# Kernel tuning notes

Hardware: AMD Instinct MI355X
Metric: run time of the kernel (lower is better)

Reference implementation:

```python
import jax, jax.numpy as jnp
import numpy as np

N = 50000      # nodes
K = 32         # fixed neighbor count per node
D_IN, D_HID, D_OUT = 512, 128, 64


def setup_inputs() -> dict:
    key = jax.random.key(0)
    k1, k2, k3, k4 = jax.random.split(key, 4)
    feat = jax.random.normal(k1, (N, D_IN), dtype=jnp.float32)
    W1 = jax.random.normal(k2, (D_IN, D_HID), dtype=jnp.float32) * (1.0 / np.sqrt(D_IN))
    b1 = jnp.zeros((D_HID,), dtype=jnp.float32)
    W2 = jax.random.normal(k3, (D_HID, D_OUT), dtype=jnp.float32) * (1.0 / np.sqrt(D_HID))
    b2 = jnp.zeros((D_OUT,), dtype=jnp.float32)
    neighbors = jax.random.randint(k4, (N, K), 0, N, dtype=jnp.int64)
    return {"feat": feat, "W1": W1, "b1": b1, "W2": W2, "b2": b2,
            "neighbors": neighbors}


def _median_conv(x, W, b, neighbors):
    # linear transform, then per-node median over neighbor messages
    h = x @ W + b                      # [N, D]
    nb = h[neighbors]                  # [N, K, D]  gather (irregular access)
    # torch.median returns the lower middle element for even K
    med = jnp.sort(nb, axis=1)[:, (K - 1) // 2]   # [N, D]
    return med


def reference(feat, W1, b1, W2, b2, neighbors):
    # MedianGCN forward (eval mode: dropout is identity), norm='none'
    h = jax.nn.relu(_median_conv(feat, W1, b1, neighbors))
    out = _median_conv(h, W2, b2, neighbors)
    return out
```

## Files before the change

### kernel.cpp

```cpp
#include <hip/hip_runtime.h>
#include <cstddef>

#define NN   50000
#define KNB  32

typedef _Float16 h2    __attribute__((ext_vector_type(2)));
typedef _Float16 half8 __attribute__((ext_vector_type(8)));
typedef float    f4    __attribute__((ext_vector_type(4)));
typedef float    f8    __attribute__((ext_vector_type(8)));

__global__ __launch_bounds__(256) void prep(const float* __restrict__ W1,
                                            const float* __restrict__ W2,
                                            _Float16* __restrict__ w1t,
                                            _Float16* __restrict__ w2t) {
  const int id = blockIdx.x * 256 + threadIdx.x;
  if (id < 128 * 512) {
    const int n = id >> 9, k = id & 511;
    w1t[id] = (_Float16)W1[k * 128 + n];
  } else {
    const int id2 = id - 128 * 512;
    if (id2 < 64 * 128) {
      const int n = id2 >> 7, k = id2 & 127;
      w2t[id2] = (_Float16)W2[k * 64 + n];
    }
  }
}

__global__ __launch_bounds__(256) void gemm1_mfma(
    const float* __restrict__ A, const _Float16* __restrict__ Bt,
    const float* __restrict__ bias, _Float16* __restrict__ C, int M) {
  constexpr int K = 512, BM = 64, BK = 32;
  __shared__ _Float16 Ah[BM][40];
  __shared__ _Float16 Bh[128][40];
  const int tid  = threadIdx.x;
  const int wave = tid >> 6;
  const int lane = tid & 63;
  const int mr   = lane & 15;
  const int kg   = lane >> 4;
  const int m0   = blockIdx.x * BM;

  const int srow = tid >> 2;
  const int sseg = (tid & 3) * 8;
  int aRow = m0 + srow;
  if (aRow >= M) aRow = M - 1;
  const float*    ap  = A  + (size_t)aRow * K + sseg;
  const _Float16* bp0 = Bt + (size_t)srow * K + sseg;
  const _Float16* bp1 = Bt + (size_t)(64 + srow) * K + sseg;

  f4 acc[8] = {};

  for (int k0 = 0; k0 < K; k0 += BK) {
    const f4 t0 = *(const f4*)ap;
    const f4 t1 = *(const f4*)(ap + 4);
    const half8 blo = *(const half8*)bp0;
    const half8 bhi = *(const half8*)bp1;
    const f8 av = {t0[0], t0[1], t0[2], t0[3], t1[0], t1[1], t1[2], t1[3]};
    *(half8*)&Ah[srow][sseg]      = __builtin_convertvector(av, half8);
    *(half8*)&Bh[srow][sseg]      = blo;
    *(half8*)&Bh[64 + srow][sseg] = bhi;
    __syncthreads();

    const half8 af = *(const half8*)&Ah[wave * 16 + mr][kg * 8];
    #pragma unroll
    for (int nt = 0; nt < 8; ++nt) {
      const half8 bf = *(const half8*)&Bh[nt * 16 + mr][kg * 8];
      acc[nt] = __builtin_amdgcn_mfma_f32_16x16x32_f16(af, bf, acc[nt], 0, 0, 0);
    }
    __syncthreads();
    ap += BK;
    bp0 += BK;
    bp1 += BK;
  }

  #pragma unroll
  for (int nt = 0; nt < 8; ++nt) {
    const int col = nt * 16 + mr;
    const float bv = bias[col];
    #pragma unroll
    for (int r = 0; r < 4; ++r) {
      const int row = m0 + wave * 16 + kg * 4 + r;
      if (row < M)
        C[(size_t)row * 128 + col] = (_Float16)(acc[nt][r] + bv);
    }
  }
}

__global__ __launch_bounds__(256) void gemm2_mfma(
    const _Float16* __restrict__ A, const _Float16* __restrict__ Bt,
    const float* __restrict__ bias, _Float16* __restrict__ C, int M) {
  constexpr int K = 128, BM = 64, BK = 32;
  __shared__ _Float16 Ah[BM][40];
  __shared__ _Float16 Bh[64][40];
  const int tid  = threadIdx.x;
  const int wave = tid >> 6;
  const int lane = tid & 63;
  const int mr   = lane & 15;
  const int kg   = lane >> 4;
  const int m0   = blockIdx.x * BM;

  const int srow = tid >> 2;
  const int sseg = (tid & 3) * 8;
  int aRow = m0 + srow;
  if (aRow >= M) aRow = M - 1;
  const _Float16* ap = A  + (size_t)aRow * K + sseg;
  const _Float16* bp = Bt + (size_t)srow * K + sseg;

  f4 acc[4] = {};

  #pragma unroll
  for (int k0 = 0; k0 < K; k0 += BK) {
    *(half8*)&Ah[srow][sseg] = *(const half8*)ap;
    *(half8*)&Bh[srow][sseg] = *(const half8*)bp;
    __syncthreads();

    const half8 af = *(const half8*)&Ah[wave * 16 + mr][kg * 8];
    #pragma unroll
    for (int nt = 0; nt < 4; ++nt) {
      const half8 bf = *(const half8*)&Bh[nt * 16 + mr][kg * 8];
      acc[nt] = __builtin_amdgcn_mfma_f32_16x16x32_f16(af, bf, acc[nt], 0, 0, 0);
    }
    __syncthreads();
    ap += BK;
    bp += BK;
  }

  #pragma unroll
  for (int nt = 0; nt < 4; ++nt) {
    const int col = nt * 16 + mr;
    const float bv = bias[col];
    #pragma unroll
    for (int r = 0; r < 4; ++r) {
      const int row = m0 + wave * 16 + kg * 4 + r;
      if (row < M)
        C[(size_t)row * 64 + col] = (_Float16)(acc[nt][r] + bv);
    }
  }
}

__device__ __forceinline__ void ceh(h2& a, h2& b) {
  h2 lo = __builtin_elementwise_min(a, b);
  h2 hi = __builtin_elementwise_max(a, b);
  a = lo;
  b = hi;
}

__device__ __forceinline__ void sort32h(h2 (&v)[32]) {
  #pragma unroll
  for (int p = 1; p < 32; p <<= 1) {
    #pragma unroll
    for (int k = p; k >= 1; k >>= 1) {
      #pragma unroll
      for (int j = k & (p - 1); j + k < 32; j += 2 * k) {
        #pragma unroll
        for (int i = 0; i < k; ++i) {
          if (i + j + k < 32) {
            if ((i + j) / (2 * p) == (i + j + k) / (2 * p)) {
              ceh(v[i + j], v[i + j + k]);
            }
          }
        }
      }
    }
  }
}

__global__ __launch_bounds__(256) void median_relu1(const h2* __restrict__ H,
                                                    const int* __restrict__ nb,
                                                    h2* __restrict__ O) {
  const int node = blockIdx.x * 4 + (threadIdx.x >> 6);
  const int lane = threadIdx.x & 63;
  const int* nrow = nb + (size_t)node * KNB;
  h2 v[32];
  #pragma unroll
  for (int j = 0; j < KNB; ++j) {
    const int idx = nrow[j];
    v[j] = H[(size_t)idx * 64 + lane];
  }
  sort32h(v);
  const h2 z = (h2)((_Float16)0);
  O[(size_t)node * 64 + lane] = __builtin_elementwise_max(v[15], z);
}

__global__ __launch_bounds__(256) void median2(const h2* __restrict__ H,
                                               const int* __restrict__ nb,
                                               float2* __restrict__ O) {
  const int node = blockIdx.x * 8 + (threadIdx.x >> 5);
  const int lane = threadIdx.x & 31;
  const int* nrow = nb + (size_t)node * KNB;
  h2 v[32];
  #pragma unroll
  for (int j = 0; j < KNB; ++j) {
    const int idx = nrow[j];
    v[j] = H[(size_t)idx * 32 + lane];
  }
  sort32h(v);
  float2 o;
  o.x = (float)v[15][0];
  o.y = (float)v[15][1];
  O[(size_t)node * 32 + lane] = o;
}

extern "C" void kernel_launch(void* const* d_in, const int* in_sizes, int n_in,
                              void* d_out, int out_size, void* d_ws, size_t ws_size,
                              hipStream_t stream) {
  const float* feat = (const float*)d_in[0];
  const float* W1   = (const float*)d_in[1];
  const float* b1   = (const float*)d_in[2];
  const float* W2   = (const float*)d_in[3];
  const float* b2   = (const float*)d_in[4];
  const int*   nb   = (const int*)d_in[5];
  float* out = (float*)d_out;

  _Float16* h1   = (_Float16*)d_ws;
  _Float16* med1 = h1 + (size_t)NN * 128;
  _Float16* w1t  = med1 + (size_t)NN * 128;
  _Float16* w2t  = w1t + 128 * 512;
  _Float16* h2b  = h1;

  prep<<<dim3(288), dim3(256), 0, stream>>>(W1, W2, w1t, w2t);
  gemm1_mfma<<<dim3((NN + 63) / 64), dim3(256), 0, stream>>>(feat, w1t, b1, h1, NN);
  median_relu1<<<dim3(NN / 4), dim3(256), 0, stream>>>(
      (const h2*)h1, nb, (h2*)med1);
  gemm2_mfma<<<dim3((NN + 63) / 64), dim3(256), 0, stream>>>(med1, w2t, b2, h2b, NN);
  median2<<<dim3(NN / 8), dim3(256), 0, stream>>>(
      (const h2*)h2b, nb, (float2*)out);
}
```

Baseline: 257.6 us.

## Store hidden features in column-chunked layout and use 16-bit neighbor indices

The GEMM outputs are written in a chunked layout, with 16 features per chunk stored contiguously per node, so each median block gathers from one 1.6MB chunk slice. This is meant to improve cache locality of the random neighbor gathers. Neighbor indices are also compacted to 16-bit by a new prep kernel and staged in shared memory per block of 32 nodes. Node ids up to 50000 fit in an unsigned 16-bit value. The cost is an extra kernel launch, strided A loads in gemm2, and narrower 32-byte gather segments per node.

```diff
diff --git a/kernel.cpp b/kernel.cpp
--- a/kernel.cpp
+++ b/kernel.cpp
@@ -3,11 +3,13 @@
 
 #define NN   50000
 #define KNB  32
+#define NBLK ((NN + 31) / 32)
 
 typedef _Float16 h2    __attribute__((ext_vector_type(2)));
 typedef _Float16 half8 __attribute__((ext_vector_type(8)));
 typedef float    f4    __attribute__((ext_vector_type(4)));
 typedef float    f8    __attribute__((ext_vector_type(8)));
+typedef unsigned short ushort_t;
 
 __global__ __launch_bounds__(256) void prep(const float* __restrict__ W1,
                                             const float* __restrict__ W2,
@@ -26,9 +28,21 @@
   }
 }
 
+__global__ __launch_bounds__(256) void prepnb(const int* __restrict__ nb,
+                                              ushort_t* __restrict__ nb16) {
+  const int i = (blockIdx.x * 256 + threadIdx.x) * 4;
+  if (i + 3 < NN * KNB) {
+    const int4 v = *(const int4*)(nb + i);
+    ushort4 u;
+    u.x = (ushort_t)v.x; u.y = (ushort_t)v.y;
+    u.z = (ushort_t)v.z; u.w = (ushort_t)v.w;
+    *(ushort4*)(nb16 + i) = u;
+  }
+}
+
 __global__ __launch_bounds__(256) void gemm1_mfma(
     const float* __restrict__ A, const _Float16* __restrict__ Bt,
-    const float* __restrict__ bias, _Float16* __restrict__ C, int M) {
+    const float* __restrict__ bias, _Float16* __restrict__ h1c, int M) {
   constexpr int K = 512, BM = 64, BK = 32;
   __shared__ _Float16 Ah[BM][40];
   __shared__ _Float16 Bh[128][40];
@@ -74,20 +88,19 @@
 
   #pragma unroll
   for (int nt = 0; nt < 8; ++nt) {
-    const int col = nt * 16 + mr;
-    const float bv = bias[col];
+    const float bv = bias[nt * 16 + mr];
     #pragma unroll
     for (int r = 0; r < 4; ++r) {
       const int row = m0 + wave * 16 + kg * 4 + r;
       if (row < M)
-        C[(size_t)row * 128 + col] = (_Float16)(acc[nt][r] + bv);
+        h1c[((size_t)nt * NN + row) * 16 + mr] = (_Float16)(acc[nt][r] + bv);
     }
   }
 }
 
 __global__ __launch_bounds__(256) void gemm2_mfma(
-    const _Float16* __restrict__ A, const _Float16* __restrict__ Bt,
-    const float* __restrict__ bias, _Float16* __restrict__ C, int M) {
+    const _Float16* __restrict__ med1c, const _Float16* __restrict__ Bt,
+    const float* __restrict__ bias, _Float16* __restrict__ h2c, int M) {
   constexpr int K = 128, BM = 64, BK = 32;
   __shared__ _Float16 Ah[BM][40];
   __shared__ _Float16 Bh[64][40];
@@ -102,13 +115,15 @@
   const int sseg = (tid & 3) * 8;
   int aRow = m0 + srow;
   if (aRow >= M) aRow = M - 1;
-  const _Float16* ap = A  + (size_t)aRow * K + sseg;
   const _Float16* bp = Bt + (size_t)srow * K + sseg;
 
   f4 acc[4] = {};
 
   #pragma unroll
   for (int k0 = 0; k0 < K; k0 += BK) {
+    const int kk = k0 + sseg;
+    const _Float16* ap =
+        med1c + ((size_t)(kk >> 4) * NN + aRow) * 16 + (kk & 15);
     *(half8*)&Ah[srow][sseg] = *(const half8*)ap;
     *(half8*)&Bh[srow][sseg] = *(const half8*)bp;
     __syncthreads();
@@ -120,19 +135,17 @@
       acc[nt] = __builtin_amdgcn_mfma_f32_16x16x32_f16(af, bf, acc[nt], 0, 0, 0);
     }
     __syncthreads();
-    ap += BK;
     bp += BK;
   }
 
   #pragma unroll
   for (int nt = 0; nt < 4; ++nt) {
-    const int col = nt * 16 + mr;
-    const float bv = bias[col];
+    const float bv = bias[nt * 16 + mr];
     #pragma unroll
     for (int r = 0; r < 4; ++r) {
       const int row = m0 + wave * 16 + kg * 4 + r;
       if (row < M)
-        C[(size_t)row * 64 + col] = (_Float16)(acc[nt][r] + bv);
+        h2c[((size_t)nt * NN + row) * 16 + mr] = (_Float16)(acc[nt][r] + bv);
     }
   }
 }
@@ -164,40 +177,73 @@
   }
 }
 
-__global__ __launch_bounds__(256) void median_relu1(const h2* __restrict__ H,
-                                                    const int* __restrict__ nb,
-                                                    h2* __restrict__ O) {
-  const int node = blockIdx.x * 4 + (threadIdx.x >> 6);
-  const int lane = threadIdx.x & 63;
-  const int* nrow = nb + (size_t)node * KNB;
+__global__ __launch_bounds__(256) void median_relu1c(
+    const h2* __restrict__ h1c, const ushort_t* __restrict__ nb16,
+    h2* __restrict__ med1c) {
+  const int c   = blockIdx.x / NBLK;
+  const int nb0 = (blockIdx.x % NBLK) * 32;
+  const int tid = threadIdx.x;
+  __shared__ ushort_t sidx[32 * KNB];
+
+  {
+    const int gi = nb0 * KNB + tid * 4;
+    ushort4 u = make_ushort4(0, 0, 0, 0);
+    if (gi + 3 < NN * KNB) u = *(const ushort4*)(nb16 + gi);
+    *(ushort4*)(sidx + tid * 4) = u;
+  }
+  __syncthreads();
+
+  const int nloc = tid >> 3;
+  const int f2   = tid & 7;
+  const int node = nb0 + nloc;
+  const h2* src = h1c + (size_t)c * NN * 8;
+
   h2 v[32];
   #pragma unroll
   for (int j = 0; j < KNB; ++j) {
-    const int idx = nrow[j];
-    v[j] = H[(size_t)idx * 64 + lane];
+    const int idx = sidx[nloc * KNB + j];
+    v[j] = src[(size_t)idx * 8 + f2];
   }
   sort32h(v);
   const h2 z = (h2)((_Float16)0);
-  O[(size_t)node * 64 + lane] = __builtin_elementwise_max(v[15], z);
-}
-
-__global__ __launch_bounds__(256) void median2(const h2* __restrict__ H,
-                                               const int* __restrict__ nb,
-                                               float2* __restrict__ O) {
-  const int node = blockIdx.x * 8 + (threadIdx.x >> 5);
-  const int lane = threadIdx.x & 31;
-  const int* nrow = nb + (size_t)node * KNB;
+  if (node < NN)
+    med1c[((size_t)c * NN + node) * 8 + f2] = __builtin_elementwise_max(v[15], z);
+}
+
+__global__ __launch_bounds__(256) void median2c(
+    const h2* __restrict__ h2c, const ushort_t* __restrict__ nb16,
+    float2* __restrict__ O) {
+  const int c   = blockIdx.x / NBLK;
+  const int nb0 = (blockIdx.x % NBLK) * 32;
+  const int tid = threadIdx.x;
+  __shared__ ushort_t sidx[32 * KNB];
+
+  {
+    const int gi = nb0 * KNB + tid * 4;
+    ushort4 u = make_ushort4(0, 0, 0, 0);
+    if (gi + 3 < NN * KNB) u = *(const ushort4*)(nb16 + gi);
+    *(ushort4*)(sidx + tid * 4) = u;
+  }
+  __syncthreads();
+
+  const int nloc = tid >> 3;
+  const int f2   = tid & 7;
+  const int node = nb0 + nloc;
+  const h2* src = h2c + (size_t)c * NN * 8;
+
   h2 v[32];
   #pragma unroll
   for (int j = 0; j < KNB; ++j) {
-    const int idx = nrow[j];
-    v[j] = H[(size_t)idx * 32 + lane];
+    const int idx = sidx[nloc * KNB + j];
+    v[j] = src[(size_t)idx * 8 + f2];
   }
   sort32h(v);
-  float2 o;
-  o.x = (float)v[15][0];
-  o.y = (float)v[15][1];
-  O[(size_t)node * 32 + lane] = o;
+  if (node < NN) {
+    float2 o;
+    o.x = (float)v[15][0];
+    o.y = (float)v[15][1];
+    O[(size_t)node * 32 + c * 8 + f2] = o;
+  }
 }
 
 extern "C" void kernel_launch(void* const* d_in, const int* in_sizes, int n_in,
@@ -211,17 +257,19 @@
   const int*   nb   = (const int*)d_in[5];
   float* out = (float*)d_out;
 
-  _Float16* h1   = (_Float16*)d_ws;
-  _Float16* med1 = h1 + (size_t)NN * 128;
-  _Float16* w1t  = med1 + (size_t)NN * 128;
-  _Float16* w2t  = w1t + 128 * 512;
-  _Float16* h2b  = h1;
+  _Float16* h1c   = (_Float16*)d_ws;
+  _Float16* med1c = h1c + (size_t)NN * 128;
+  _Float16* w1t   = med1c + (size_t)NN * 128;
+  _Float16* w2t   = w1t + 128 * 512;
+  ushort_t* nb16  = (ushort_t*)(w2t + 64 * 128);
+  _Float16* h2c   = h1c;
 
   prep<<<dim3(288), dim3(256), 0, stream>>>(W1, W2, w1t, w2t);
-  gemm1_mfma<<<dim3((NN + 63) / 64), dim3(256), 0, stream>>>(feat, w1t, b1, h1, NN);
-  median_relu1<<<dim3(NN / 4), dim3(256), 0, stream>>>(
-      (const h2*)h1, nb, (h2*)med1);
-  gemm2_mfma<<<dim3((NN + 63) / 64), dim3(256), 0, stream>>>(med1, w2t, b2, h2b, NN);
-  median2<<<dim3(NN / 8), dim3(256), 0, stream>>>(
-      (const h2*)h2b, nb, (float2*)out);
-}
+  prepnb<<<dim3((NN * KNB / 4 + 255) / 256), dim3(256), 0, stream>>>(nb, nb16);
+  gemm1_mfma<<<dim3((NN + 63) / 64), dim3(256), 0, stream>>>(feat, w1t, b1, h1c, NN);
+  median_relu1c<<<dim3(8 * NBLK), dim3(256), 0, stream>>>(
+      (const h2*)h1c, nb16, (h2*)med1c);
+  gemm2_mfma<<<dim3((NN + 63) / 64), dim3(256), 0, stream>>>(med1c, w2t, b2, h2c, NN);
+  median2c<<<dim3(4 * NBLK), dim3(256), 0, stream>>>(
+      (const h2*)h2c, nb16, (float2*)out);
+}
```

Measured after the change: 283.4 us. +10.0%, slower.
